# Optimization experiments

Hardware: AMD Instinct MI355X
Metric: run time of the kernel (lower is better)

Reference implementation:

```python
import jax, jax.numpy as jnp
import numpy as np

N, E, CIN, H, B, NCOV, NCLASS, T = 50000, 800000, 64, 64, 256, 8, 2, 3


def setup_inputs() -> dict:
    key = jax.random.key(0)
    ks = jax.random.split(key, 24)
    s = 1.0 / np.sqrt(H)
    nrm = lambda k, shp, sc: (jax.random.normal(k, shp, jnp.float32) * sc)
    p = {}
    p["x"] = nrm(ks[0], (N, 3 * CIN), 1.0)
    p["edge_index"] = jax.random.randint(ks[1], (2, E), 0, N)
    p["cov"] = nrm(ks[2], (B, NCOV), 1.0)
    p["batch"] = jnp.sort(jax.random.randint(ks[3], (N,), 0, B))
    p["h0"] = nrm(ks[4], (B, H), 1.0)
    p["c0"] = nrm(ks[5], (B, H), 1.0)
    # GCNEncoder params (shared across the 3 channel slices, as in the torch code)
    p["lin_W"] = nrm(ks[6], (CIN, H), s)
    p["lin_b"] = jnp.zeros((H,), jnp.float32)
    p["conv1_W"] = nrm(ks[7], (H, H), s)
    p["conv1_b"] = jnp.zeros((H,), jnp.float32)
    p["conv2_W"] = nrm(ks[8], (H, H), s)
    p["conv2_b"] = jnp.zeros((H,), jnp.float32)
    # LSTM (1 layer), torch gate order i,f,g,o
    p["Wih"] = nrm(ks[9], (4 * H, H), s)
    p["Whh"] = nrm(ks[10], (4 * H, H), s)
    p["bih"] = jnp.zeros((4 * H,), jnp.float32)
    p["bhh"] = jnp.zeros((4 * H,), jnp.float32)
    p["w0_W"] = nrm(ks[11], (H, H), s)
    p["w0_b"] = jnp.zeros((H,), jnp.float32)
    p["attn_W"] = nrm(ks[12], (1, H), s)
    p["attn_b"] = jnp.zeros((1,), jnp.float32)
    p["l1_W"] = nrm(ks[13], (8, H), s)
    p["l1_b"] = jnp.zeros((8,), jnp.float32)
    p["l2_W"] = nrm(ks[14], (NCLASS, 8 + NCOV), 1.0 / np.sqrt(8 + NCOV))
    p["l2_b"] = jnp.zeros((NCLASS,), jnp.float32)
    return p


def _gcn_conv(x, src, dst, dinv, W, b):
    xw = x @ W
    norm = dinv[src] * dinv[dst]                      # [E]
    agg = jax.ops.segment_sum(norm[:, None] * xw[src], dst, num_segments=N)
    agg = agg + (2.0 * dinv * dinv)[:, None] * xw     # self-loop (weight 2)
    return agg + b


def _encoder(x, src, dst, dinv, lin_W, lin_b, c1W, c1b, c2W, c2b):
    out = x @ lin_W + lin_b                           # dropout = identity (eval)
    out1 = jax.nn.relu(_gcn_conv(out, src, dst, dinv, c1W, c1b)) + out
    out2 = _gcn_conv(out1, src, dst, dinv, c2W, c2b) + out1
    return out2


def reference(x, edge_index, cov, batch, h0, c0, lin_W, lin_b, conv1_W, conv1_b,
              conv2_W, conv2_b, Wih, Whh, bih, bhh, w0_W, w0_b, attn_W, attn_b,
              l1_W, l1_b, l2_W, l2_b):
    src, dst = edge_index[0], edge_index[1]
    deg = jax.ops.segment_sum(jnp.ones((E,), jnp.float32), dst, num_segments=N) + 2.0
    dinv = jax.lax.rsqrt(deg)
    enc = lambda xi: _encoder(xi, src, dst, dinv, lin_W, lin_b,
                              conv1_W, conv1_b, conv2_W, conv2_b)
    o1 = enc(x[:, :CIN]); o2 = enc(x[:, CIN:2 * CIN]); o3 = enc(x[:, 2 * CIN:])
    # global_mean_pool per branch
    cnt = jnp.maximum(jax.ops.segment_sum(jnp.ones((N,), jnp.float32), batch,
                                          num_segments=B), 1.0)[:, None]
    pool = lambda o: jax.ops.segment_sum(o, batch, num_segments=B) / cnt
    seq = jnp.stack([pool(o1), pool(o2), pool(o3)], axis=1)  # [B, 3, H]

    # 1-layer LSTM over T=3 (torch gate order i,f,g,o)
    def step(carry, x_t):
        h, c = carry
        g = x_t @ Wih.T + bih + h @ Whh.T + bhh
        i, f, gg, o = jnp.split(g, 4, axis=-1)
        c = jax.nn.sigmoid(f) * c + jax.nn.sigmoid(i) * jnp.tanh(gg)
        h = jax.nn.sigmoid(o) * jnp.tanh(c)
        return (h, c), h

    (_, _), hs = jax.lax.scan(step, (h0, c0), jnp.swapaxes(seq, 0, 1))
    rnn_out = jnp.swapaxes(hs, 0, 1)                         # [B, T, H]
    r = jnp.tanh(rnn_out @ w0_W.T + w0_b)
    attn = jax.nn.softmax((r @ attn_W.T + attn_b)[..., 0], axis=1)  # [B, T]
    pooled = jnp.einsum('bth,bt->bh', r, attn)
    out = jax.nn.relu(pooled @ l1_W.T + l1_b)
    out = jnp.concatenate([out, cov], axis=1)
    out = out @ l2_W.T + l2_b
    return attn, out
```

## Files before the change

kernel.cpp:

```cpp
#include <hip/hip_runtime.h>
#include <math.h>


#define TT 3
#define CHUNK 2048
#define BCAP 16384

typedef __attribute__((ext_vector_type(2))) float floatx2;

__device__ __forceinline__ float sigmoidf_(float x) { return 1.f / (1.f + expf(-x)); }
__device__ __forceinline__ float bf2f(unsigned short u) {
    return __uint_as_float((unsigned)u << 16);
}
__device__ __forceinline__ unsigned short f2bf(float f) {
    unsigned u = __float_as_uint(f);
    u += 0x7FFFu + ((u >> 16) & 1u);
    return (unsigned short)(u >> 16);
}

__global__ void brow_sorted(const int* __restrict__ batch, int* __restrict__ brow,
                            int* __restrict__ bcnt, int N, int B) {
    if (blockIdx.x == 0) bcnt[threadIdx.x] = 0;
    int n = blockIdx.x * 256 + threadIdx.x;
    if (n >= N) return;
    int b = batch[n];
    if (n == 0) {
        for (int q = 0; q <= b; ++q) brow[q] = 0;
    } else {
        int pb = batch[n - 1];
        for (int q = pb + 1; q <= b; ++q) brow[q] = n;
    }
    if (n == N - 1) {
        for (int q = b + 1; q <= B; ++q) brow[q] = N;
    }
}

__global__ void stage_direct(const int* __restrict__ src, const int* __restrict__ dst,
                             int* __restrict__ bcnt, unsigned* __restrict__ stg, int E) {
    __shared__ int hcnt[256], hbase[256], hcur[256];
    hcnt[threadIdx.x] = 0;
    __syncthreads();
    int base = blockIdx.x * CHUNK;
    for (int i = threadIdx.x; i < CHUNK; i += 256) {
        int e = base + i;
        if (e < E) atomicAdd(&hcnt[dst[e] >> 8], 1);
    }
    __syncthreads();
    int c = hcnt[threadIdx.x];
    if (c) hbase[threadIdx.x] = atomicAdd(&bcnt[threadIdx.x], c);
    hcur[threadIdx.x] = 0;
    __syncthreads();
    for (int i = threadIdx.x; i < CHUNK; i += 256) {
        int e = base + i;
        if (e < E) {
            int d = dst[e];
            int b = d >> 8;
            int r = atomicAdd(&hcur[b], 1);
            stg[(long)b * BCAP + hbase[b] + r] =
                (unsigned)src[e] | ((unsigned)(d & 255) << 24);
        }
    }
}

__global__ void bucket_build(const unsigned* __restrict__ stg, const int* __restrict__ bcnt,
                             int* __restrict__ rowptr, float* __restrict__ dinv,
                             int* __restrict__ csrc, int nb, int N, int E) {
    const int b = blockIdx.x;
    const int n0 = b << 8;
    __shared__ int cnt[256];
    __shared__ int pfx[256];
    __shared__ int boffb_sh;
    int bv = (threadIdx.x < nb) ? bcnt[threadIdx.x] : 0;
    pfx[threadIdx.x] = bv;
    __syncthreads();
    for (int off = 1; off < 256; off <<= 1) {
        int t = (threadIdx.x >= off) ? pfx[threadIdx.x - off] : 0;
        __syncthreads();
        pfx[threadIdx.x] += t;
        __syncthreads();
    }
    if (threadIdx.x == b) boffb_sh = pfx[threadIdx.x] - bv;
    cnt[threadIdx.x] = 0;
    __syncthreads();
    const int boffb = boffb_sh;

    const long s = (long)b * BCAP;
    const long e = s + bcnt[b];
    for (long p = s + threadIdx.x; p < e; p += 256)
        atomicAdd(&cnt[stg[p] >> 24], 1);
    __syncthreads();
    int v = cnt[threadIdx.x];
    pfx[threadIdx.x] = v;
    __syncthreads();
    for (int off = 1; off < 256; off <<= 1) {
        int t = (threadIdx.x >= off) ? pfx[threadIdx.x - off] : 0;
        __syncthreads();
        pfx[threadIdx.x] += t;
        __syncthreads();
    }
    int rowbase = boffb + pfx[threadIdx.x] - v;
    int n = n0 + threadIdx.x;
    if (n < N) {
        rowptr[n] = rowbase;
        dinv[n] = rsqrtf((float)v + 2.0f);
    }
    if (b == 0 && threadIdx.x == 0) rowptr[N] = E;
    cnt[threadIdx.x] = rowbase;
    __syncthreads();
    for (long p = s + threadIdx.x; p < e; p += 256) {
        unsigned u = stg[p];
        int dl = u >> 24;
        int r = atomicAdd(&cnt[dl], 1);
        csrc[r] = (int)(u & 0xFFFFFFu);
    }
}

__global__ __launch_bounds__(256) void gemm_lin(
    const float* __restrict__ x, const float* __restrict__ W,
    const float* __restrict__ bias, unsigned short* __restrict__ C,
    long cStride, int nrows) {
    __shared__ float AT[64][68];
    __shared__ float Ws[64][68];
    const int t = threadIdx.x;
    const int r0 = blockIdx.x * 64;

    #pragma unroll
    for (int i = 0; i < 4; ++i) {
        int idx = t + i * 256;
        int k = idx >> 4, c4 = idx & 15;
        *(float4*)&Ws[k][c4 * 4] = *(const float4*)(W + k * 64 + c4 * 4);
    }
    #pragma unroll
    for (int i = 0; i < 4; ++i) {
        int idx = t + i * 256;
        int row = idx >> 4, c4 = idx & 15;
        int gr = r0 + row;
        float4 a = make_float4(0.f, 0.f, 0.f, 0.f);
        if (gr < nrows)
            a = *(const float4*)(x + (long)gr * 192 + blockIdx.y * 64 + c4 * 4);
        AT[c4 * 4 + 0][row] = a.x;
        AT[c4 * 4 + 1][row] = a.y;
        AT[c4 * 4 + 2][row] = a.z;
        AT[c4 * 4 + 3][row] = a.w;
    }
    __syncthreads();

    const int rowg = t >> 4, colg = t & 15;
    float acc[4][4] = {};
    #pragma unroll 8
    for (int k = 0; k < 64; ++k) {
        float4 av = *(const float4*)&AT[k][rowg * 4];
        float4 wv = *(const float4*)&Ws[k][colg * 4];
        #pragma unroll
        for (int i = 0; i < 4; ++i) {
            acc[i][0] = fmaf(((const float*)&av)[i], wv.x, acc[i][0]);
            acc[i][1] = fmaf(((const float*)&av)[i], wv.y, acc[i][1]);
            acc[i][2] = fmaf(((const float*)&av)[i], wv.z, acc[i][2]);
            acc[i][3] = fmaf(((const float*)&av)[i], wv.w, acc[i][3]);
        }
    }
    float b0 = bias[colg * 4 + 0], b1 = bias[colg * 4 + 1];
    float b2 = bias[colg * 4 + 2], b3 = bias[colg * 4 + 3];
    unsigned short* Cb = C + (long)blockIdx.y * cStride;
    #pragma unroll
    for (int i = 0; i < 4; ++i) {
        int gr = r0 + rowg * 4 + i;
        if (gr < nrows) {
            ushort4 o;
            o.x = f2bf(acc[i][0] + b0); o.y = f2bf(acc[i][1] + b1);
            o.z = f2bf(acc[i][2] + b2); o.w = f2bf(acc[i][3] + b3);
            *(ushort4*)(Cb + (long)gr * 64 + colg * 4) = o;
        }
    }
}

__global__ __launch_bounds__(256) void gemm_t8(
    const unsigned short* __restrict__ A, long aStride, const float* __restrict__ W,
    unsigned* __restrict__ T8, const float* __restrict__ dinvp, int nrows) {
    __shared__ float AT[64][68];
    __shared__ float Ws[64][68];
    const int t = threadIdx.x;
    const unsigned short* Ab = A + (long)blockIdx.y * aStride;
    const int r0 = blockIdx.x * 64;

    #pragma unroll
    for (int i = 0; i < 4; ++i) {
        int idx = t + i * 256;
        int k = idx >> 4, c4 = idx & 15;
        *(float4*)&Ws[k][c4 * 4] = *(const float4*)(W + k * 64 + c4 * 4);
    }
    #pragma unroll
    for (int i = 0; i < 4; ++i) {
        int idx = t + i * 256;
        int row = idx >> 4, c4 = idx & 15;
        int gr = r0 + row;
        ushort4 a = make_ushort4(0, 0, 0, 0);
        if (gr < nrows) a = *(const ushort4*)(Ab + (long)gr * 64 + c4 * 4);
        AT[c4 * 4 + 0][row] = bf2f(a.x);
        AT[c4 * 4 + 1][row] = bf2f(a.y);
        AT[c4 * 4 + 2][row] = bf2f(a.z);
        AT[c4 * 4 + 3][row] = bf2f(a.w);
    }
    __syncthreads();

    const int rowg = t >> 4, colg = t & 15;
    float acc[4][4] = {};
    #pragma unroll 8
    for (int k = 0; k < 64; ++k) {
        float4 av = *(const float4*)&AT[k][rowg * 4];
        float4 wv = *(const float4*)&Ws[k][colg * 4];
        #pragma unroll
        for (int i = 0; i < 4; ++i) {
            acc[i][0] = fmaf(((const float*)&av)[i], wv.x, acc[i][0]);
            acc[i][1] = fmaf(((const float*)&av)[i], wv.y, acc[i][1]);
            acc[i][2] = fmaf(((const float*)&av)[i], wv.z, acc[i][2]);
            acc[i][3] = fmaf(((const float*)&av)[i], wv.w, acc[i][3]);
        }
    }
    #pragma unroll
    for (int i = 0; i < 4; ++i) {
        int gr = r0 + rowg * 4 + i;
        if (gr >= nrows) continue;
        float sc = dinvp[gr];
        int r = 0;
        r = __builtin_amdgcn_cvt_pk_fp8_f32(acc[i][0] * sc, acc[i][1] * sc, r, false);
        r = __builtin_amdgcn_cvt_pk_fp8_f32(acc[i][2] * sc, acc[i][3] * sc, r, true);
        T8[(long)gr * 48 + blockIdx.y * 16 + colg] = (unsigned)r;
    }
}

#define EDGE3(uu)                                                        \
    {                                                                    \
        floatx2 lo = __builtin_amdgcn_cvt_pk_f32_fp8(uu, false);         \
        floatx2 hi = __builtin_amdgcn_cvt_pk_f32_fp8(uu, true);          \
        a0[ch] += lo.x; a1[ch] += lo.y; a2[ch] += hi.x; a3[ch] += hi.y;  \
    }

template <bool RELU>
__global__ __launch_bounds__(256) void gcn_gather3_f8(
    const int* __restrict__ rowptr, const int* __restrict__ csrc,
    const float* __restrict__ dinv, const unsigned* __restrict__ tc,
    const float* __restrict__ bias, const unsigned short* __restrict__ prev, long chS,
    unsigned short* __restrict__ outp, int N) {
    long gid = ((long)blockIdx.x * 256 + threadIdx.x) >> 4;
    int n = (int)gid;
    if (n >= N) return;
    const int jj = threadIdx.x & 15;

    const int end = rowptr[n + 1];
    const float din = dinv[n];
    float a0[TT] = {}, a1[TT] = {}, a2[TT] = {}, a3[TT] = {};
    int p = rowptr[n];
    for (; p + 3 < end; p += 4) {
        long r0 = (long)csrc[p]     * 48 + jj;
        long r1 = (long)csrc[p + 1] * 48 + jj;
        long r2 = (long)csrc[p + 2] * 48 + jj;
        long r3 = (long)csrc[p + 3] * 48 + jj;
        #pragma unroll
        for (int ch = 0; ch < TT; ++ch) {
            unsigned u0 = tc[r0 + ch * 16];
            unsigned u1 = tc[r1 + ch * 16];
            unsigned u2 = tc[r2 + ch * 16];
            unsigned u3 = tc[r3 + ch * 16];
            EDGE3(u0) EDGE3(u1) EDGE3(u2) EDGE3(u3)
        }
    }
    for (; p < end; ++p) {
        long r = (long)csrc[p] * 48 + jj;
        #pragma unroll
        for (int ch = 0; ch < TT; ++ch) {
            unsigned u = tc[r + ch * 16];
            EDGE3(u)
        }
    }
    float4 bv = *(const float4*)(bias + 4 * jj);
    long nrow = (long)n * 48 + jj;
    long off = (long)n * 64 + 4 * jj;
    #pragma unroll
    for (int ch = 0; ch < TT; ++ch) {
        unsigned us = tc[nrow + ch * 16];
        floatx2 slo = __builtin_amdgcn_cvt_pk_f32_fp8(us, false);
        floatx2 shi = __builtin_amdgcn_cvt_pk_f32_fp8(us, true);
        float v0 = (a0[ch] + 2.f * slo.x) * din + bv.x;
        float v1 = (a1[ch] + 2.f * slo.y) * din + bv.y;
        float v2 = (a2[ch] + 2.f * shi.x) * din + bv.z;
        float v3 = (a3[ch] + 2.f * shi.y) * din + bv.w;
        if (RELU) {
            v0 = fmaxf(v0, 0.f); v1 = fmaxf(v1, 0.f);
            v2 = fmaxf(v2, 0.f); v3 = fmaxf(v3, 0.f);
        }
        ushort4 pv = *(const ushort4*)(prev + ch * chS + off);
        ushort4 o;
        o.x = f2bf(v0 + bf2f(pv.x));
        o.y = f2bf(v1 + bf2f(pv.y));
        o.z = f2bf(v2 + bf2f(pv.z));
        o.w = f2bf(v3 + bf2f(pv.w));
        *(ushort4*)(outp + ch * chS + off) = o;
    }
}

__global__ __launch_bounds__(256) void head_fused(
    const unsigned short* __restrict__ out2, long chS, const int* __restrict__ brow,
    const float* __restrict__ h0, const float* __restrict__ c0,
    const float* __restrict__ Wih, const float* __restrict__ Whh,
    const float* __restrict__ bih, const float* __restrict__ bhh,
    const float* __restrict__ w0W, const float* __restrict__ w0b,
    const float* __restrict__ attnW, const float* __restrict__ attnb,
    const float* __restrict__ l1W, const float* __restrict__ l1b,
    const float* __restrict__ l2W, const float* __restrict__ l2b,
    const float* __restrict__ cov, float* __restrict__ out_attn,
    float* __restrict__ out_cls) {
    const int b = blockIdx.x;
    const int t = threadIdx.x;

    __shared__ float x[TT][64];
    __shared__ float h[64], c[64];
    __shared__ float gates[256];
    __shared__ float rnn[TT][64];
    __shared__ float r[TT][64];
    __shared__ float logit[TT];
    __shared__ float a[TT];
    __shared__ float pooled[64];
    __shared__ float l1o[16];

    const int s = brow[b], e = brow[b + 1];
    float inv = 1.0f / fmaxf((float)(e - s), 1.0f);
    if (t < TT * 64) {
        int ch = t >> 6, j = t & 63;
        const unsigned short* p = out2 + (long)ch * chS + j;
        float acc = 0.f;
        for (int n = s; n < e; ++n) acc += bf2f(p[(long)n * 64]);
        x[ch][j] = acc * inv;
    }
    if (t < 64) { h[t] = h0[(long)b * 64 + t]; c[t] = c0[(long)b * 64 + t]; }
    __syncthreads();

    for (int step = 0; step < TT; ++step) {
        float g = bih[t] + bhh[t];
        const float* wi = Wih + (long)t * 64;
        const float* wh = Whh + (long)t * 64;
        #pragma unroll 8
        for (int k = 0; k < 64; ++k) g += wi[k] * x[step][k] + wh[k] * h[k];
        gates[t] = g;
        __syncthreads();
        if (t < 64) {
            float ig = sigmoidf_(gates[t]);
            float fg = sigmoidf_(gates[64 + t]);
            float gg = tanhf(gates[128 + t]);
            float og = sigmoidf_(gates[192 + t]);
            float cn = fg * c[t] + ig * gg;
            c[t] = cn;
            float hn = og * tanhf(cn);
            h[t] = hn;
            rnn[step][t] = hn;
        }
        __syncthreads();
    }

    if (t < TT * 64) {
        int tt = t / 64, j = t % 64;
        float v = w0b[j];
        const float* wr = w0W + (long)j * 64;
        #pragma unroll 8
        for (int k = 0; k < 64; ++k) v += rnn[tt][k] * wr[k];
        r[tt][j] = tanhf(v);
    }
    __syncthreads();

    if (t < TT) {
        float v = attnb[0];
        #pragma unroll 8
        for (int k = 0; k < 64; ++k) v += r[t][k] * attnW[k];
        logit[t] = v;
    }
    __syncthreads();

    if (t == 0) {
        float m = fmaxf(logit[0], fmaxf(logit[1], logit[2]));
        float e0 = expf(logit[0] - m), e1 = expf(logit[1] - m), e2 = expf(logit[2] - m);
        float sm = e0 + e1 + e2;
        a[0] = e0 / sm; a[1] = e1 / sm; a[2] = e2 / sm;
        out_attn[(long)b * TT + 0] = a[0];
        out_attn[(long)b * TT + 1] = a[1];
        out_attn[(long)b * TT + 2] = a[2];
    }
    __syncthreads();

    if (t < 64) pooled[t] = a[0] * r[0][t] + a[1] * r[1][t] + a[2] * r[2][t];
    __syncthreads();

    if (t < 8) {
        float v = l1b[t];
        const float* w = l1W + (long)t * 64;
        #pragma unroll 8
        for (int k = 0; k < 64; ++k) v += pooled[k] * w[k];
        l1o[t] = fmaxf(v, 0.f);
    } else if (t < 16) {
        l1o[t] = cov[(long)b * 8 + (t - 8)];
    }
    __syncthreads();

    if (t < 2) {
        float v = l2b[t];
        const float* w = l2W + (long)t * 16;
        #pragma unroll
        for (int k = 0; k < 16; ++k) v += l1o[k] * w[k];
        out_cls[(long)b * 2 + t] = v;
    }
}

extern "C" void kernel_launch(void* const* d_in, const int* in_sizes, int n_in,
                              void* d_out, int out_size, void* d_ws, size_t ws_size,
                              hipStream_t stream) {
    const float* x       = (const float*)d_in[0];
    const int*   eidx    = (const int*)d_in[1];
    const float* cov     = (const float*)d_in[2];
    const int*   batch   = (const int*)d_in[3];
    const float* h0      = (const float*)d_in[4];
    const float* c0      = (const float*)d_in[5];
    const float* lin_W   = (const float*)d_in[6];
    const float* lin_b   = (const float*)d_in[7];
    const float* conv1_W = (const float*)d_in[8];
    const float* conv1_b = (const float*)d_in[9];
    const float* conv2_W = (const float*)d_in[10];
    const float* conv2_b = (const float*)d_in[11];
    const float* Wih     = (const float*)d_in[12];
    const float* Whh     = (const float*)d_in[13];
    const float* bih     = (const float*)d_in[14];
    const float* bhh     = (const float*)d_in[15];
    const float* w0_W    = (const float*)d_in[16];
    const float* w0_b    = (const float*)d_in[17];
    const float* attn_W  = (const float*)d_in[18];
    const float* attn_b  = (const float*)d_in[19];
    const float* l1_W    = (const float*)d_in[20];
    const float* l1_b    = (const float*)d_in[21];
    const float* l2_W    = (const float*)d_in[22];
    const float* l2_b    = (const float*)d_in[23];

    const int N = in_sizes[3];
    const int E = in_sizes[1] / 2;
    const int B = in_sizes[2] / 8;

    const int* src = eidx;
    const int* dst = eidx + E;

    auto cdiv = [](long a, long b) { return (int)((a + b - 1) / b); };
    const int nb = cdiv(N, 256);

    char* w = (char*)d_ws;
    float* dinv   = (float*)w;  w += (size_t)N * 4;
    int*   rowptr = (int*)w;    w += (size_t)(N + 1) * 4;
    int*   brow   = (int*)w;    w += (size_t)(B + 1) * 4;
    int*   bcnt   = (int*)w;    w += 256 * 4;
    int*   csrc   = (int*)w;    w += (size_t)E * 4;
    unsigned* stg = (unsigned*)w; w += (size_t)nb * BCAP * 4;
    unsigned short* buf0 = (unsigned short*)w;  w += (size_t)TT * N * 64 * 2;
    unsigned short* bufA = (unsigned short*)w;  w += (size_t)TT * N * 64 * 2;
    unsigned* tb8 = (unsigned*)w;  w += (size_t)N * 48 * 4;
    const long chS = (long)N * 64;

    float* out_attn = (float*)d_out;
    float* out_cls  = out_attn + (long)B * TT;

    brow_sorted<<<cdiv(N, 256), 256, 0, stream>>>(batch, brow, bcnt, N, B);
    stage_direct<<<cdiv(E, CHUNK), 256, 0, stream>>>(src, dst, bcnt, stg, E);
    bucket_build<<<nb, 256, 0, stream>>>(stg, bcnt, rowptr, dinv, csrc, nb, N, E);

    const int gemm_gx = cdiv(N, 64);
    const int ng_gx   = cdiv((long)N * 16, 256);

    {
        dim3 ggrid(gemm_gx, TT);
        gemm_lin<<<ggrid, 256, 0, stream>>>(x, lin_W, lin_b, buf0, chS, N);
    }
    {
        dim3 ggrid(gemm_gx, TT);
        gemm_t8<<<ggrid, 256, 0, stream>>>(buf0, chS, conv1_W, tb8, dinv, N);
    }
    gcn_gather3_f8<true><<<ng_gx, 256, 0, stream>>>(
        rowptr, csrc, dinv, tb8, conv1_b, buf0, chS, bufA, N);
    {
        dim3 ggrid(gemm_gx, TT);
        gemm_t8<<<ggrid, 256, 0, stream>>>(bufA, chS, conv2_W, tb8, dinv, N);
    }
    gcn_gather3_f8<false><<<ng_gx, 256, 0, stream>>>(
        rowptr, csrc, dinv, tb8, conv2_b, bufA, chS, buf0, N);

    head_fused<<<B, 256, 0, stream>>>(buf0, chS, brow, h0, c0, Wih, Whh, bih, bhh,
                                      w0_W, w0_b, attn_W, attn_b, l1_W, l1_b,
                                      l2_W, l2_b, cov, out_attn, out_cls);
}
```

Baseline: 258.9 us.

## Fuse all stages into one cooperative persistent kernel with grid syncs

Replaces the eight separate kernel launches (CSR build, GEMMs, gathers, head) with a single cooperative kernel whose phases are separated by grid-wide syncs. Blocks loop over the former grid indices persistently, and a new seq buffer is allocated for pooled features. The aim is to remove launch gaps and inter-kernel idle time. In exchange it adds grid barriers, caps occupancy through launch bounds, and gives the fused shared-memory union and register pressure to every phase.

```diff
diff --git a/kernel.cpp b/kernel.cpp
--- a/kernel.cpp
+++ b/kernel.cpp
@@ -1,10 +1,13 @@
 #include <hip/hip_runtime.h>
+#include <hip/hip_cooperative_groups.h>
 #include <math.h>
 
 
 #define TT 3
 #define CHUNK 2048
 #define BCAP 16384
+
+namespace cg = cooperative_groups;
 
 typedef __attribute__((ext_vector_type(2))) float floatx2;
 
@@ -18,117 +21,39 @@
     return (unsigned short)(u >> 16);
 }
 
-__global__ void brow_sorted(const int* __restrict__ batch, int* __restrict__ brow,
-                            int* __restrict__ bcnt, int N, int B) {
-    if (blockIdx.x == 0) bcnt[threadIdx.x] = 0;
-    int n = blockIdx.x * 256 + threadIdx.x;
-    if (n >= N) return;
-    int b = batch[n];
-    if (n == 0) {
-        for (int q = 0; q <= b; ++q) brow[q] = 0;
-    } else {
-        int pb = batch[n - 1];
-        for (int q = pb + 1; q <= b; ++q) brow[q] = n;
-    }
-    if (n == N - 1) {
-        for (int q = b + 1; q <= B; ++q) brow[q] = N;
-    }
-}
-
-__global__ void stage_direct(const int* __restrict__ src, const int* __restrict__ dst,
-                             int* __restrict__ bcnt, unsigned* __restrict__ stg, int E) {
-    __shared__ int hcnt[256], hbase[256], hcur[256];
-    hcnt[threadIdx.x] = 0;
-    __syncthreads();
-    int base = blockIdx.x * CHUNK;
-    for (int i = threadIdx.x; i < CHUNK; i += 256) {
-        int e = base + i;
-        if (e < E) atomicAdd(&hcnt[dst[e] >> 8], 1);
-    }
-    __syncthreads();
-    int c = hcnt[threadIdx.x];
-    if (c) hbase[threadIdx.x] = atomicAdd(&bcnt[threadIdx.x], c);
-    hcur[threadIdx.x] = 0;
-    __syncthreads();
-    for (int i = threadIdx.x; i < CHUNK; i += 256) {
-        int e = base + i;
-        if (e < E) {
-            int d = dst[e];
-            int b = d >> 8;
-            int r = atomicAdd(&hcur[b], 1);
-            stg[(long)b * BCAP + hbase[b] + r] =
-                (unsigned)src[e] | ((unsigned)(d & 255) << 24);
-        }
-    }
-}
-
-__global__ void bucket_build(const unsigned* __restrict__ stg, const int* __restrict__ bcnt,
-                             int* __restrict__ rowptr, float* __restrict__ dinv,
-                             int* __restrict__ csrc, int nb, int N, int E) {
-    const int b = blockIdx.x;
-    const int n0 = b << 8;
-    __shared__ int cnt[256];
-    __shared__ int pfx[256];
-    __shared__ int boffb_sh;
-    int bv = (threadIdx.x < nb) ? bcnt[threadIdx.x] : 0;
-    pfx[threadIdx.x] = bv;
-    __syncthreads();
-    for (int off = 1; off < 256; off <<= 1) {
-        int t = (threadIdx.x >= off) ? pfx[threadIdx.x - off] : 0;
-        __syncthreads();
-        pfx[threadIdx.x] += t;
-        __syncthreads();
-    }
-    if (threadIdx.x == b) boffb_sh = pfx[threadIdx.x] - bv;
-    cnt[threadIdx.x] = 0;
-    __syncthreads();
-    const int boffb = boffb_sh;
-
-    const long s = (long)b * BCAP;
-    const long e = s + bcnt[b];
-    for (long p = s + threadIdx.x; p < e; p += 256)
-        atomicAdd(&cnt[stg[p] >> 24], 1);
-    __syncthreads();
-    int v = cnt[threadIdx.x];
-    pfx[threadIdx.x] = v;
-    __syncthreads();
-    for (int off = 1; off < 256; off <<= 1) {
-        int t = (threadIdx.x >= off) ? pfx[threadIdx.x - off] : 0;
-        __syncthreads();
-        pfx[threadIdx.x] += t;
-        __syncthreads();
-    }
-    int rowbase = boffb + pfx[threadIdx.x] - v;
-    int n = n0 + threadIdx.x;
-    if (n < N) {
-        rowptr[n] = rowbase;
-        dinv[n] = rsqrtf((float)v + 2.0f);
-    }
-    if (b == 0 && threadIdx.x == 0) rowptr[N] = E;
-    cnt[threadIdx.x] = rowbase;
-    __syncthreads();
-    for (long p = s + threadIdx.x; p < e; p += 256) {
-        unsigned u = stg[p];
-        int dl = u >> 24;
-        int r = atomicAdd(&cnt[dl], 1);
-        csrc[r] = (int)(u & 0xFFFFFFu);
-    }
-}
-
-__global__ __launch_bounds__(256) void gemm_lin(
-    const float* __restrict__ x, const float* __restrict__ W,
-    const float* __restrict__ bias, unsigned short* __restrict__ C,
-    long cStride, int nrows) {
-    __shared__ float AT[64][68];
-    __shared__ float Ws[64][68];
+struct GNNParams {
+    const float* x; const int* src; const int* dst; const int* batch;
+    const float* cov; const float* h0; const float* c0;
+    const float* linW; const float* linb;
+    const float* c1W; const float* c1b;
+    const float* c2W; const float* c2b;
+    const float* Wih; const float* Whh; const float* bih; const float* bhh;
+    const float* w0W; const float* w0b; const float* attnW; const float* attnb;
+    const float* l1W; const float* l1b; const float* l2W; const float* l2b;
+    float* dinv; int* rowptr; int* brow; int* bcnt; int* csrc; unsigned* stg;
+    float* seq; unsigned short* buf0; unsigned short* bufA; unsigned* tb8;
+    float* out_attn; float* out_cls;
+    int N, E, B, nb, gemm_gx, ng_total;
+    long chS;
+};
+
+struct SmemGemm  { float AT[64][68]; float Ws[64][68]; };
+struct SmemStage { int hcnt[256], hbase[256], hcur[256]; };
+struct SmemBuild { int cnt[256], pfx[256], boffb; };
+struct SmemPool  { float part[4][64]; };
+struct SmemHead  {
+    float x[TT][64], h[64], c[64], gates[256], rnn[TT][64], r[TT][64];
+    float logit[TT], a[TT], pooled[64], l1o[16];
+};
+
+__device__ void gemm_lin_body(const GNNParams& P, SmemGemm& s, int bx, int ch) {
     const int t = threadIdx.x;
-    const int r0 = blockIdx.x * 64;
-
+    const int r0 = bx * 64;
     #pragma unroll
     for (int i = 0; i < 4; ++i) {
         int idx = t + i * 256;
         int k = idx >> 4, c4 = idx & 15;
-        *(float4*)&Ws[k][c4 * 4] = *(const float4*)(W + k * 64 + c4 * 4);
+        *(float4*)&s.Ws[k][c4 * 4] = *(const float4*)(P.linW + k * 64 + c4 * 4);
     }
     #pragma unroll
     for (int i = 0; i < 4; ++i) {
@@ -136,21 +61,20 @@
         int row = idx >> 4, c4 = idx & 15;
         int gr = r0 + row;
         float4 a = make_float4(0.f, 0.f, 0.f, 0.f);
-        if (gr < nrows)
-            a = *(const float4*)(x + (long)gr * 192 + blockIdx.y * 64 + c4 * 4);
-        AT[c4 * 4 + 0][row] = a.x;
-        AT[c4 * 4 + 1][row] = a.y;
-        AT[c4 * 4 + 2][row] = a.z;
-        AT[c4 * 4 + 3][row] = a.w;
+        if (gr < P.N)
+            a = *(const float4*)(P.x + (long)gr * 192 + ch * 64 + c4 * 4);
+        s.AT[c4 * 4 + 0][row] = a.x;
+        s.AT[c4 * 4 + 1][row] = a.y;
+        s.AT[c4 * 4 + 2][row] = a.z;
+        s.AT[c4 * 4 + 3][row] = a.w;
     }
     __syncthreads();
-
     const int rowg = t >> 4, colg = t & 15;
     float acc[4][4] = {};
     #pragma unroll 8
     for (int k = 0; k < 64; ++k) {
-        float4 av = *(const float4*)&AT[k][rowg * 4];
-        float4 wv = *(const float4*)&Ws[k][colg * 4];
+        float4 av = *(const float4*)&s.AT[k][rowg * 4];
+        float4 wv = *(const float4*)&s.Ws[k][colg * 4];
         #pragma unroll
         for (int i = 0; i < 4; ++i) {
             acc[i][0] = fmaf(((const float*)&av)[i], wv.x, acc[i][0]);
@@ -159,13 +83,13 @@
             acc[i][3] = fmaf(((const float*)&av)[i], wv.w, acc[i][3]);
         }
     }
-    float b0 = bias[colg * 4 + 0], b1 = bias[colg * 4 + 1];
-    float b2 = bias[colg * 4 + 2], b3 = bias[colg * 4 + 3];
-    unsigned short* Cb = C + (long)blockIdx.y * cStride;
+    float b0 = P.linb[colg * 4 + 0], b1 = P.linb[colg * 4 + 1];
+    float b2 = P.linb[colg * 4 + 2], b3 = P.linb[colg * 4 + 3];
+    unsigned short* Cb = P.buf0 + (long)ch * P.chS;
     #pragma unroll
     for (int i = 0; i < 4; ++i) {
         int gr = r0 + rowg * 4 + i;
-        if (gr < nrows) {
+        if (gr < P.N) {
             ushort4 o;
             o.x = f2bf(acc[i][0] + b0); o.y = f2bf(acc[i][1] + b1);
             o.z = f2bf(acc[i][2] + b2); o.w = f2bf(acc[i][3] + b3);
@@ -174,20 +98,17 @@
     }
 }
 
-__global__ __launch_bounds__(256) void gemm_t8(
-    const unsigned short* __restrict__ A, long aStride, const float* __restrict__ W,
-    unsigned* __restrict__ T8, const float* __restrict__ dinvp, int nrows) {
-    __shared__ float AT[64][68];
-    __shared__ float Ws[64][68];
+__device__ void gemm_t8_body(const GNNParams& P, SmemGemm& s,
+                             const unsigned short* A, const float* W,
+                             int bx, int ch) {
     const int t = threadIdx.x;
-    const unsigned short* Ab = A + (long)blockIdx.y * aStride;
-    const int r0 = blockIdx.x * 64;
-
+    const unsigned short* Ab = A + (long)ch * P.chS;
+    const int r0 = bx * 64;
     #pragma unroll
     for (int i = 0; i < 4; ++i) {
         int idx = t + i * 256;
         int k = idx >> 4, c4 = idx & 15;
-        *(float4*)&Ws[k][c4 * 4] = *(const float4*)(W + k * 64 + c4 * 4);
+        *(float4*)&s.Ws[k][c4 * 4] = *(const float4*)(W + k * 64 + c4 * 4);
     }
     #pragma unroll
     for (int i = 0; i < 4; ++i) {
@@ -195,20 +116,19 @@
         int row = idx >> 4, c4 = idx & 15;
         int gr = r0 + row;
         ushort4 a = make_ushort4(0, 0, 0, 0);
-        if (gr < nrows) a = *(const ushort4*)(Ab + (long)gr * 64 + c4 * 4);
-        AT[c4 * 4 + 0][row] = bf2f(a.x);
-        AT[c4 * 4 + 1][row] = bf2f(a.y);
-        AT[c4 * 4 + 2][row] = bf2f(a.z);
-        AT[c4 * 4 + 3][row] = bf2f(a.w);
+        if (gr < P.N) a = *(const ushort4*)(Ab + (long)gr * 64 + c4 * 4);
+        s.AT[c4 * 4 + 0][row] = bf2f(a.x);
+        s.AT[c4 * 4 + 1][row] = bf2f(a.y);
+        s.AT[c4 * 4 + 2][row] = bf2f(a.z);
+        s.AT[c4 * 4 + 3][row] = bf2f(a.w);
     }
     __syncthreads();
-
     const int rowg = t >> 4, colg = t & 15;
     float acc[4][4] = {};
     #pragma unroll 8
     for (int k = 0; k < 64; ++k) {
-        float4 av = *(const float4*)&AT[k][rowg * 4];
-        float4 wv = *(const float4*)&Ws[k][colg * 4];
+        float4 av = *(const float4*)&s.AT[k][rowg * 4];
+        float4 wv = *(const float4*)&s.Ws[k][colg * 4];
         #pragma unroll
         for (int i = 0; i < 4; ++i) {
             acc[i][0] = fmaf(((const float*)&av)[i], wv.x, acc[i][0]);
@@ -220,12 +140,12 @@
     #pragma unroll
     for (int i = 0; i < 4; ++i) {
         int gr = r0 + rowg * 4 + i;
-        if (gr >= nrows) continue;
-        float sc = dinvp[gr];
+        if (gr >= P.N) continue;
+        float sc = P.dinv[gr];
         int r = 0;
         r = __builtin_amdgcn_cvt_pk_fp8_f32(acc[i][0] * sc, acc[i][1] * sc, r, false);
         r = __builtin_amdgcn_cvt_pk_fp8_f32(acc[i][2] * sc, acc[i][3] * sc, r, true);
-        T8[(long)gr * 48 + blockIdx.y * 16 + colg] = (unsigned)r;
+        P.tb8[(long)gr * 48 + ch * 16 + colg] = (unsigned)r;
     }
 }
 
@@ -236,21 +156,19 @@
         a0[ch] += lo.x; a1[ch] += lo.y; a2[ch] += hi.x; a3[ch] += hi.y;  \
     }
 
-template <bool RELU>
-__global__ __launch_bounds__(256) void gcn_gather3_f8(
-    const int* __restrict__ rowptr, const int* __restrict__ csrc,
-    const float* __restrict__ dinv, const unsigned* __restrict__ tc,
-    const float* __restrict__ bias, const unsigned short* __restrict__ prev, long chS,
-    unsigned short* __restrict__ outp, int N) {
-    long gid = ((long)blockIdx.x * 256 + threadIdx.x) >> 4;
+__device__ void gather_body(const GNNParams& P, const float* bias,
+                            const unsigned short* prev, unsigned short* outp,
+                            bool relu, int vb) {
+    long gid = ((long)vb * 256 + threadIdx.x) >> 4;
     int n = (int)gid;
-    if (n >= N) return;
+    if (n >= P.N) return;
     const int jj = threadIdx.x & 15;
-
-    const int end = rowptr[n + 1];
-    const float din = dinv[n];
+    const unsigned* tc = P.tb8;
+    const int* csrc = P.csrc;
+    const int end = P.rowptr[n + 1];
+    const float din = P.dinv[n];
     float a0[TT] = {}, a1[TT] = {}, a2[TT] = {}, a3[TT] = {};
-    int p = rowptr[n];
+    int p = P.rowptr[n];
     for (; p + 3 < end; p += 4) {
         long r0 = (long)csrc[p]     * 48 + jj;
         long r1 = (long)csrc[p + 1] * 48 + jj;
@@ -285,208 +203,328 @@
         float v1 = (a1[ch] + 2.f * slo.y) * din + bv.y;
         float v2 = (a2[ch] + 2.f * shi.x) * din + bv.z;
         float v3 = (a3[ch] + 2.f * shi.y) * din + bv.w;
-        if (RELU) {
+        if (relu) {
             v0 = fmaxf(v0, 0.f); v1 = fmaxf(v1, 0.f);
             v2 = fmaxf(v2, 0.f); v3 = fmaxf(v3, 0.f);
         }
-        ushort4 pv = *(const ushort4*)(prev + ch * chS + off);
+        ushort4 pv = *(const ushort4*)(prev + ch * P.chS + off);
         ushort4 o;
         o.x = f2bf(v0 + bf2f(pv.x));
         o.y = f2bf(v1 + bf2f(pv.y));
         o.z = f2bf(v2 + bf2f(pv.z));
         o.w = f2bf(v3 + bf2f(pv.w));
-        *(ushort4*)(outp + ch * chS + off) = o;
-    }
-}
-
-__global__ __launch_bounds__(256) void head_fused(
-    const unsigned short* __restrict__ out2, long chS, const int* __restrict__ brow,
-    const float* __restrict__ h0, const float* __restrict__ c0,
-    const float* __restrict__ Wih, const float* __restrict__ Whh,
-    const float* __restrict__ bih, const float* __restrict__ bhh,
-    const float* __restrict__ w0W, const float* __restrict__ w0b,
-    const float* __restrict__ attnW, const float* __restrict__ attnb,
-    const float* __restrict__ l1W, const float* __restrict__ l1b,
-    const float* __restrict__ l2W, const float* __restrict__ l2b,
-    const float* __restrict__ cov, float* __restrict__ out_attn,
-    float* __restrict__ out_cls) {
-    const int b = blockIdx.x;
+        *(ushort4*)(outp + ch * P.chS + off) = o;
+    }
+}
+
+__global__ __launch_bounds__(256, 4) void mega(GNNParams P) {
+    cg::grid_group g = cg::this_grid();
+    __shared__ __align__(16) char sm[sizeof(SmemGemm)];
     const int t = threadIdx.x;
 
-    __shared__ float x[TT][64];
-    __shared__ float h[64], c[64];
-    __shared__ float gates[256];
-    __shared__ float rnn[TT][64];
-    __shared__ float r[TT][64];
-    __shared__ float logit[TT];
-    __shared__ float a[TT];
-    __shared__ float pooled[64];
-    __shared__ float l1o[16];
-
-    const int s = brow[b], e = brow[b + 1];
-    float inv = 1.0f / fmaxf((float)(e - s), 1.0f);
-    if (t < TT * 64) {
-        int ch = t >> 6, j = t & 63;
-        const unsigned short* p = out2 + (long)ch * chS + j;
-        float acc = 0.f;
-        for (int n = s; n < e; ++n) acc += bf2f(p[(long)n * 64]);
-        x[ch][j] = acc * inv;
-    }
-    if (t < 64) { h[t] = h0[(long)b * 64 + t]; c[t] = c0[(long)b * 64 + t]; }
-    __syncthreads();
-
-    for (int step = 0; step < TT; ++step) {
-        float g = bih[t] + bhh[t];
-        const float* wi = Wih + (long)t * 64;
-        const float* wh = Whh + (long)t * 64;
-        #pragma unroll 8
-        for (int k = 0; k < 64; ++k) g += wi[k] * x[step][k] + wh[k] * h[k];
-        gates[t] = g;
-        __syncthreads();
-        if (t < 64) {
-            float ig = sigmoidf_(gates[t]);
-            float fg = sigmoidf_(gates[64 + t]);
-            float gg = tanhf(gates[128 + t]);
-            float og = sigmoidf_(gates[192 + t]);
-            float cn = fg * c[t] + ig * gg;
-            c[t] = cn;
-            float hn = og * tanhf(cn);
-            h[t] = hn;
-            rnn[step][t] = hn;
-        }
-        __syncthreads();
-    }
-
-    if (t < TT * 64) {
-        int tt = t / 64, j = t % 64;
-        float v = w0b[j];
-        const float* wr = w0W + (long)j * 64;
-        #pragma unroll 8
-        for (int k = 0; k < 64; ++k) v += rnn[tt][k] * wr[k];
-        r[tt][j] = tanhf(v);
-    }
-    __syncthreads();
-
-    if (t < TT) {
-        float v = attnb[0];
-        #pragma unroll 8
-        for (int k = 0; k < 64; ++k) v += r[t][k] * attnW[k];
-        logit[t] = v;
-    }
-    __syncthreads();
-
-    if (t == 0) {
-        float m = fmaxf(logit[0], fmaxf(logit[1], logit[2]));
-        float e0 = expf(logit[0] - m), e1 = expf(logit[1] - m), e2 = expf(logit[2] - m);
-        float sm = e0 + e1 + e2;
-        a[0] = e0 / sm; a[1] = e1 / sm; a[2] = e2 / sm;
-        out_attn[(long)b * TT + 0] = a[0];
-        out_attn[(long)b * TT + 1] = a[1];
-        out_attn[(long)b * TT + 2] = a[2];
-    }
-    __syncthreads();
-
-    if (t < 64) pooled[t] = a[0] * r[0][t] + a[1] * r[1][t] + a[2] * r[2][t];
-    __syncthreads();
-
-    if (t < 8) {
-        float v = l1b[t];
-        const float* w = l1W + (long)t * 64;
-        #pragma unroll 8
-        for (int k = 0; k < 64; ++k) v += pooled[k] * w[k];
-        l1o[t] = fmaxf(v, 0.f);
-    } else if (t < 16) {
-        l1o[t] = cov[(long)b * 8 + (t - 8)];
-    }
-    __syncthreads();
-
-    if (t < 2) {
-        float v = l2b[t];
-        const float* w = l2W + (long)t * 16;
-        #pragma unroll
-        for (int k = 0; k < 16; ++k) v += l1o[k] * w[k];
-        out_cls[(long)b * 2 + t] = v;
+    if (blockIdx.x == 0) P.bcnt[t] = 0;
+    for (long n = (long)blockIdx.x * 256 + t; n < P.N; n += (long)gridDim.x * 256) {
+        int b = P.batch[n];
+        if (n == 0) {
+            for (int q = 0; q <= b; ++q) P.brow[q] = 0;
+        } else {
+            int pb = P.batch[n - 1];
+            for (int q = pb + 1; q <= b; ++q) P.brow[q] = (int)n;
+        }
+        if (n == P.N - 1) {
+            for (int q = b + 1; q <= P.B; ++q) P.brow[q] = P.N;
+        }
+    }
+    g.sync();
+
+    {
+        SmemStage& s = *reinterpret_cast<SmemStage*>(sm);
+        int nchunks = (P.E + CHUNK - 1) / CHUNK;
+        for (int cb = blockIdx.x; cb < nchunks; cb += gridDim.x) {
+            __syncthreads();
+            s.hcnt[t] = 0;
+            __syncthreads();
+            int base = cb * CHUNK;
+            for (int i = t; i < CHUNK; i += 256) {
+                int e = base + i;
+                if (e < P.E) atomicAdd(&s.hcnt[P.dst[e] >> 8], 1);
+            }
+            __syncthreads();
+            int c = s.hcnt[t];
+            if (c) s.hbase[t] = atomicAdd(&P.bcnt[t], c);
+            s.hcur[t] = 0;
+            __syncthreads();
+            for (int i = t; i < CHUNK; i += 256) {
+                int e = base + i;
+                if (e < P.E) {
+                    int d = P.dst[e];
+                    int b = d >> 8;
+                    int r = atomicAdd(&s.hcur[b], 1);
+                    P.stg[(long)b * BCAP + s.hbase[b] + r] =
+                        (unsigned)P.src[e] | ((unsigned)(d & 255) << 24);
+                }
+            }
+        }
+    }
+    g.sync();
+
+    {
+        SmemBuild& s = *reinterpret_cast<SmemBuild*>(sm);
+        for (int b = blockIdx.x; b < P.nb; b += gridDim.x) {
+            __syncthreads();
+            const int n0 = b << 8;
+            int bv = (t < P.nb) ? P.bcnt[t] : 0;
+            s.pfx[t] = bv;
+            __syncthreads();
+            for (int off = 1; off < 256; off <<= 1) {
+                int tv = (t >= off) ? s.pfx[t - off] : 0;
+                __syncthreads();
+                s.pfx[t] += tv;
+                __syncthreads();
+            }
+            if (t == b) s.boffb = s.pfx[t] - bv;
+            s.cnt[t] = 0;
+            __syncthreads();
+            const int boffb = s.boffb;
+            const long sbase = (long)b * BCAP;
+            const long ebase = sbase + P.bcnt[b];
+            for (long p = sbase + t; p < ebase; p += 256)
+                atomicAdd(&s.cnt[P.stg[p] >> 24], 1);
+            __syncthreads();
+            int v = s.cnt[t];
+            s.pfx[t] = v;
+            __syncthreads();
+            for (int off = 1; off < 256; off <<= 1) {
+                int tv = (t >= off) ? s.pfx[t - off] : 0;
+                __syncthreads();
+                s.pfx[t] += tv;
+                __syncthreads();
+            }
+            int rowbase = boffb + s.pfx[t] - v;
+            int n = n0 + t;
+            if (n < P.N) {
+                P.rowptr[n] = rowbase;
+                P.dinv[n] = rsqrtf((float)v + 2.0f);
+            }
+            if (b == 0 && t == 0) P.rowptr[P.N] = P.E;
+            s.cnt[t] = rowbase;
+            __syncthreads();
+            for (long p = sbase + t; p < ebase; p += 256) {
+                unsigned u = P.stg[p];
+                int dl = u >> 24;
+                int r = atomicAdd(&s.cnt[dl], 1);
+                P.csrc[r] = (int)(u & 0xFFFFFFu);
+            }
+        }
+    }
+    g.sync();
+
+    {
+        SmemGemm& s = *reinterpret_cast<SmemGemm*>(sm);
+        int total = P.gemm_gx * TT;
+        for (int vb = blockIdx.x; vb < total; vb += gridDim.x) {
+            __syncthreads();
+            gemm_lin_body(P, s, vb % P.gemm_gx, vb / P.gemm_gx);
+        }
+    }
+    g.sync();
+
+    {
+        SmemGemm& s = *reinterpret_cast<SmemGemm*>(sm);
+        int total = P.gemm_gx * TT;
+        for (int vb = blockIdx.x; vb < total; vb += gridDim.x) {
+            __syncthreads();
+            gemm_t8_body(P, s, P.buf0, P.c1W, vb % P.gemm_gx, vb / P.gemm_gx);
+        }
+    }
+    g.sync();
+
+    for (int vb = blockIdx.x; vb < P.ng_total; vb += gridDim.x)
+        gather_body(P, P.c1b, P.buf0, P.bufA, true, vb);
+    g.sync();
+
+    {
+        SmemGemm& s = *reinterpret_cast<SmemGemm*>(sm);
+        int total = P.gemm_gx * TT;
+        for (int vb = blockIdx.x; vb < total; vb += gridDim.x) {
+            __syncthreads();
+            gemm_t8_body(P, s, P.bufA, P.c2W, vb % P.gemm_gx, vb / P.gemm_gx);
+        }
+    }
+    g.sync();
+
+    for (int vb = blockIdx.x; vb < P.ng_total; vb += gridDim.x)
+        gather_body(P, P.c2b, P.bufA, P.buf0, false, vb);
+    g.sync();
+
+    {
+        SmemPool& s = *reinterpret_cast<SmemPool*>(sm);
+        int total = P.B * TT;
+        for (int vb = blockIdx.x; vb < total; vb += gridDim.x) {
+            __syncthreads();
+            int b = vb / TT, chan = vb % TT;
+            const unsigned short* srcp = P.buf0 + (long)chan * P.chS;
+            const int j = t & 63;
+            const int w = t >> 6;
+            float acc = 0.f;
+            const int sE = P.brow[b], eE = P.brow[b + 1];
+            for (int n = sE + w; n < eE; n += 4) acc += bf2f(srcp[(long)n * 64 + j]);
+            s.part[w][j] = acc;
+            __syncthreads();
+            if (w == 0)
+                P.seq[((long)b * TT + chan) * 64 + j] =
+                    s.part[0][j] + s.part[1][j] + s.part[2][j] + s.part[3][j];
+        }
+    }
+    g.sync();
+
+    {
+        SmemHead& s = *reinterpret_cast<SmemHead*>(sm);
+        for (int b = blockIdx.x; b < P.B; b += gridDim.x) {
+            __syncthreads();
+            float inv = 1.0f / fmaxf((float)(P.brow[b + 1] - P.brow[b]), 1.0f);
+            if (t < TT * 64) s.x[t / 64][t % 64] = P.seq[(long)b * TT * 64 + t] * inv;
+            if (t < 64) {
+                s.h[t] = P.h0[(long)b * 64 + t];
+                s.c[t] = P.c0[(long)b * 64 + t];
+            }
+            __syncthreads();
+            for (int step = 0; step < TT; ++step) {
+                float gg2 = P.bih[t] + P.bhh[t];
+                const float* wi = P.Wih + (long)t * 64;
+                const float* wh = P.Whh + (long)t * 64;
+                #pragma unroll 8
+                for (int k = 0; k < 64; ++k)
+                    gg2 += wi[k] * s.x[step][k] + wh[k] * s.h[k];
+                s.gates[t] = gg2;
+                __syncthreads();
+                if (t < 64) {
+                    float ig = sigmoidf_(s.gates[t]);
+                    float fg = sigmoidf_(s.gates[64 + t]);
+                    float gv = tanhf(s.gates[128 + t]);
+                    float og = sigmoidf_(s.gates[192 + t]);
+                    float cn = fg * s.c[t] + ig * gv;
+                    s.c[t] = cn;
+                    float hn = og * tanhf(cn);
+                    s.h[t] = hn;
+                    s.rnn[step][t] = hn;
+                }
+                __syncthreads();
+            }
+            if (t < TT * 64) {
+                int tt = t / 64, j = t % 64;
+                float v = P.w0b[j];
+                const float* wr = P.w0W + (long)j * 64;
+                #pragma unroll 8
+                for (int k = 0; k < 64; ++k) v += s.rnn[tt][k] * wr[k];
+                s.r[tt][j] = tanhf(v);
+            }
+            __syncthreads();
+            if (t < TT) {
+                float v = P.attnb[0];
+                #pragma unroll 8
+                for (int k = 0; k < 64; ++k) v += s.r[t][k] * P.attnW[k];
+                s.logit[t] = v;
+            }
+            __syncthreads();
+            if (t == 0) {
+                float m = fmaxf(s.logit[0], fmaxf(s.logit[1], s.logit[2]));
+                float e0 = expf(s.logit[0] - m), e1 = expf(s.logit[1] - m), e2 = expf(s.logit[2] - m);
+                float sm2 = e0 + e1 + e2;
+                s.a[0] = e0 / sm2; s.a[1] = e1 / sm2; s.a[2] = e2 / sm2;
+                P.out_attn[(long)b * TT + 0] = s.a[0];
+                P.out_attn[(long)b * TT + 1] = s.a[1];
+                P.out_attn[(long)b * TT + 2] = s.a[2];
+            }
+            __syncthreads();
+            if (t < 64)
+                s.pooled[t] = s.a[0] * s.r[0][t] + s.a[1] * s.r[1][t] + s.a[2] * s.r[2][t];
+            __syncthreads();
+            if (t < 8) {
+                float v = P.l1b[t];
+                const float* w = P.l1W + (long)t * 64;
+                #pragma unroll 8
+                for (int k = 0; k < 64; ++k) v += s.pooled[k] * w[k];
+                s.l1o[t] = fmaxf(v, 0.f);
+            } else if (t < 16) {
+                s.l1o[t] = P.cov[(long)b * 8 + (t - 8)];
+            }
+            __syncthreads();
+            if (t < 2) {
+                float v = P.l2b[t];
+                const float* w = P.l2W + (long)t * 16;
+                #pragma unroll
+                for (int k = 0; k < 16; ++k) v += s.l1o[k] * w[k];
+                P.out_cls[(long)b * 2 + t] = v;
+            }
+        }
     }
 }
 
 extern "C" void kernel_launch(void* const* d_in, const int* in_sizes, int n_in,
                               void* d_out, int out_size, void* d_ws, size_t ws_size,
                               hipStream_t stream) {
-    const float* x       = (const float*)d_in[0];
-    const int*   eidx    = (const int*)d_in[1];
-    const float* cov     = (const float*)d_in[2];
-    const int*   batch   = (const int*)d_in[3];
-    const float* h0      = (const float*)d_in[4];
-    const float* c0      = (const float*)d_in[5];
-    const float* lin_W   = (const float*)d_in[6];
-    const float* lin_b   = (const float*)d_in[7];
-    const float* conv1_W = (const float*)d_in[8];
-    const float* conv1_b = (const float*)d_in[9];
-    const float* conv2_W = (const float*)d_in[10];
-    const float* conv2_b = (const float*)d_in[11];
-    const float* Wih     = (const float*)d_in[12];
-    const float* Whh     = (const float*)d_in[13];
-    const float* bih     = (const float*)d_in[14];
-    const float* bhh     = (const float*)d_in[15];
-    const float* w0_W    = (const float*)d_in[16];
-    const float* w0_b    = (const float*)d_in[17];
-    const float* attn_W  = (const float*)d_in[18];
-    const float* attn_b  = (const float*)d_in[19];
-    const float* l1_W    = (const float*)d_in[20];
-    const float* l1_b    = (const float*)d_in[21];
-    const float* l2_W    = (const float*)d_in[22];
-    const float* l2_b    = (const float*)d_in[23];
-
-    const int N = in_sizes[3];
-    const int E = in_sizes[1] / 2;
-    const int B = in_sizes[2] / 8;
-
-    const int* src = eidx;
-    const int* dst = eidx + E;
+    GNNParams P;
+    P.x     = (const float*)d_in[0];
+    const int* eidx = (const int*)d_in[1];
+    P.cov   = (const float*)d_in[2];
+    P.batch = (const int*)d_in[3];
+    P.h0    = (const float*)d_in[4];
+    P.c0    = (const float*)d_in[5];
+    P.linW  = (const float*)d_in[6];
+    P.linb  = (const float*)d_in[7];
+    P.c1W   = (const float*)d_in[8];
+    P.c1b   = (const float*)d_in[9];
+    P.c2W   = (const float*)d_in[10];
+    P.c2b   = (const float*)d_in[11];
+    P.Wih   = (const float*)d_in[12];
+    P.Whh   = (const float*)d_in[13];
+    P.bih   = (const float*)d_in[14];
+    P.bhh   = (const float*)d_in[15];
+    P.w0W   = (const float*)d_in[16];
+    P.w0b   = (const float*)d_in[17];
+    P.attnW = (const float*)d_in[18];
+    P.attnb = (const float*)d_in[19];
+    P.l1W   = (const float*)d_in[20];
+    P.l1b   = (const float*)d_in[21];
+    P.l2W   = (const float*)d_in[22];
+    P.l2b   = (const float*)d_in[23];
+
+    P.N = in_sizes[3];
+    P.E = in_sizes[1] / 2;
+    P.B = in_sizes[2] / 8;
+    P.src = eidx;
+    P.dst = eidx + P.E;
 
     auto cdiv = [](long a, long b) { return (int)((a + b - 1) / b); };
-    const int nb = cdiv(N, 256);
+    P.nb = cdiv(P.N, 256);
+    P.gemm_gx = cdiv(P.N, 64);
+    P.ng_total = cdiv((long)P.N * 16, 256);
+    P.chS = (long)P.N * 64;
 
     char* w = (char*)d_ws;
-    float* dinv   = (float*)w;  w += (size_t)N * 4;
-    int*   rowptr = (int*)w;    w += (size_t)(N + 1) * 4;
-    int*   brow   = (int*)w;    w += (size_t)(B + 1) * 4;
-    int*   bcnt   = (int*)w;    w += 256 * 4;
-    int*   csrc   = (int*)w;    w += (size_t)E * 4;
-    unsigned* stg = (unsigned*)w; w += (size_t)nb * BCAP * 4;
-    unsigned short* buf0 = (unsigned short*)w;  w += (size_t)TT * N * 64 * 2;
-    unsigned short* bufA = (unsigned short*)w;  w += (size_t)TT * N * 64 * 2;
-    unsigned* tb8 = (unsigned*)w;  w += (size_t)N * 48 * 4;
-    const long chS = (long)N * 64;
-
-    float* out_attn = (float*)d_out;
-    float* out_cls  = out_attn + (long)B * TT;
-
-    brow_sorted<<<cdiv(N, 256), 256, 0, stream>>>(batch, brow, bcnt, N, B);
-    stage_direct<<<cdiv(E, CHUNK), 256, 0, stream>>>(src, dst, bcnt, stg, E);
-    bucket_build<<<nb, 256, 0, stream>>>(stg, bcnt, rowptr, dinv, csrc, nb, N, E);
-
-    const int gemm_gx = cdiv(N, 64);
-    const int ng_gx   = cdiv((long)N * 16, 256);
-
-    {
-        dim3 ggrid(gemm_gx, TT);
-        gemm_lin<<<ggrid, 256, 0, stream>>>(x, lin_W, lin_b, buf0, chS, N);
-    }
-    {
-        dim3 ggrid(gemm_gx, TT);
-        gemm_t8<<<ggrid, 256, 0, stream>>>(buf0, chS, conv1_W, tb8, dinv, N);
-    }
-    gcn_gather3_f8<true><<<ng_gx, 256, 0, stream>>>(
-        rowptr, csrc, dinv, tb8, conv1_b, buf0, chS, bufA, N);
-    {
-        dim3 ggrid(gemm_gx, TT);
-        gemm_t8<<<ggrid, 256, 0, stream>>>(bufA, chS, conv2_W, tb8, dinv, N);
-    }
-    gcn_gather3_f8<false><<<ng_gx, 256, 0, stream>>>(
-        rowptr, csrc, dinv, tb8, conv2_b, bufA, chS, buf0, N);
-
-    head_fused<<<B, 256, 0, stream>>>(buf0, chS, brow, h0, c0, Wih, Whh, bih, bhh,
-                                      w0_W, w0_b, attn_W, attn_b, l1_W, l1_b,
-                                      l2_W, l2_b, cov, out_attn, out_cls);
-}
+    P.dinv   = (float*)w;  w += (size_t)P.N * 4;
+    P.rowptr = (int*)w;    w += (size_t)(P.N + 1) * 4;
+    P.brow   = (int*)w;    w += (size_t)(P.B + 1) * 4;
+    P.bcnt   = (int*)w;    w += 256 * 4;
+    P.csrc   = (int*)w;    w += (size_t)P.E * 4;
+    P.stg    = (unsigned*)w; w += (size_t)P.nb * BCAP * 4;
+    P.seq    = (float*)w;  w += (size_t)P.B * TT * 64 * 4;
+    P.buf0   = (unsigned short*)w;  w += (size_t)TT * P.N * 64 * 2;
+    P.bufA   = (unsigned short*)w;  w += (size_t)TT * P.N * 64 * 2;
+    P.tb8    = (unsigned*)w;  w += (size_t)P.N * 48 * 4;
+
+    P.out_attn = (float*)d_out;
+    P.out_cls  = P.out_attn + (long)P.B * TT;
+
+    int maxPerCU = 0;
+    hipError_t qe = hipOccupancyMaxActiveBlocksPerMultiprocessor(
+        &maxPerCU, (const void*)mega, 256, 0);
+    if (qe != hipSuccess || maxPerCU < 1) maxPerCU = 2;
+    int grid = maxPerCU * 256;
+    if (grid > 2048) grid = 2048;
+
+    void* args[] = {(void*)&P};
+    hipLaunchCooperativeKernel((const void*)mega, dim3(grid), dim3(256),
+                               args, 0, stream);
+}
```

Result: slower. 777.9 us (+200.5%).
